# Performance work log

Measured on AMD Instinct MI355X. Metric: run time of the kernel, lower is better.

The kernel has to match this reference:

```python
import jax, jax.numpy as jnp
import numpy as np

N_HEADS = 16


def setup_inputs() -> dict:
    key = jax.random.key(0)
    k1, k2, k3 = jax.random.split(key, 3)
    d_model = 2048
    seq = 2048
    x = jax.random.normal(k1, (seq, d_model), dtype=jnp.float32)
    W_qkv = jax.random.normal(k2, (d_model, 3 * d_model), dtype=jnp.float32) * (d_model ** -0.5)
    b_qkv = jnp.zeros((3 * d_model,), dtype=jnp.float32)
    W_out = jax.random.normal(k3, (d_model, d_model), dtype=jnp.float32) * (d_model ** -0.5)
    b_out = jnp.zeros((d_model,), dtype=jnp.float32)
    return {"x": x, "W_qkv": W_qkv, "b_qkv": b_qkv, "W_out": W_out, "b_out": b_out}


def reference(x, W_qkv, b_qkv, W_out, b_out):
    seq, d_model = x.shape
    d_head = d_model // N_HEADS
    qkv = x @ W_qkv + b_qkv  # [seq, 3*d_model]
    q, k, v = jnp.split(qkv, 3, axis=1)
    # [seq, d_model] -> [n_heads, seq, d_head]
    split_heads = lambda t: t.reshape(seq, N_HEADS, d_head).transpose(1, 0, 2)
    q, k, v = split_heads(q), split_heads(k), split_heads(v)
    # NOTE: original module has NO 1/sqrt(d_head) scaling — kept faithful.
    attn = jnp.einsum('hqd,hkd->hqk', q, k)
    causal = jnp.arange(seq)[:, None] >= jnp.arange(seq)[None, :]
    attn = jnp.where(causal, attn, -jnp.inf)
    probs = jax.nn.softmax(attn, axis=-1)
    out = jnp.einsum('hqk,hkd->hqd', probs, v)  # [n_heads, seq, d_head]
    out = out.transpose(1, 0, 2).reshape(seq, d_model)
    return out @ W_out + b_out
```

## Files before the change

kernel.cpp:

```cpp
#include <hip/hip_runtime.h>
#include <stdint.h>

typedef __attribute__((ext_vector_type(8))) __bf16 bf16x8;
typedef __attribute__((ext_vector_type(4))) float  f32x4;

#define MFMA16(A, B, C) __builtin_amdgcn_mfma_f32_16x16x32_bf16((A), (B), (C), 0, 0, 0)

__device__ __forceinline__ unsigned short f2b(float f) {
  union { float f; uint32_t u; } c; c.f = f;
  uint32_t u = c.u;
  u += 0x7fffu + ((u >> 16) & 1u);
  return (unsigned short)(u >> 16);
}
__device__ __forceinline__ float b2f(unsigned short s) {
  union { uint32_t u; float f; } c; c.u = ((uint32_t)s) << 16;
  return c.f;
}
__device__ __forceinline__ void async_cp16(const void* g, void* l) {
  __builtin_amdgcn_global_load_lds((const __attribute__((address_space(1))) uint32_t*)g,
                                   (__attribute__((address_space(3))) uint32_t*)l, 16, 0, 0);
}

__global__ __launch_bounds__(256) void split_hi_lo(const float* __restrict__ in,
                                                   unsigned short* __restrict__ hi,
                                                   unsigned short* __restrict__ lo, int n4) {
  int i = blockIdx.x * 256 + threadIdx.x;
  if (i >= n4) return;
  const float4 v = ((const float4*)in)[i];
  float f[4] = {v.x, v.y, v.z, v.w};
  unsigned short hs[4], ls[4];
#pragma unroll
  for (int j = 0; j < 4; ++j) {
    hs[j] = f2b(f[j]);
    ls[j] = f2b(f[j] - b2f(hs[j]));
  }
  ((ushort4*)hi)[i] = make_ushort4(hs[0], hs[1], hs[2], hs[3]);
  ((ushort4*)lo)[i] = make_ushort4(ls[0], ls[1], ls[2], ls[3]);
}

template <int WLO>
__global__ __launch_bounds__(256) void transpose_split(const float* __restrict__ src,
                                                       unsigned short* __restrict__ dh,
                                                       unsigned short* __restrict__ dl,
                                                       int rows, int cols) {
  __shared__ float tile[64][65];
  const int r0 = blockIdx.y * 64, c0 = blockIdx.x * 64;
  const int t = threadIdx.x;
#pragma unroll
  for (int i = 0; i < 4; ++i) {
    int c = i * 256 + t;
    int rr = c >> 4, cc = (c & 15) << 2;
    const float4 v = *(const float4*)(src + (size_t)(r0 + rr) * cols + c0 + cc);
    tile[rr][cc] = v.x; tile[rr][cc + 1] = v.y; tile[rr][cc + 2] = v.z; tile[rr][cc + 3] = v.w;
  }
  __syncthreads();
#pragma unroll
  for (int i = 0; i < 4; ++i) {
    int c = i * 256 + t;
    int rr = c >> 4, cc = (c & 15) << 2;
    unsigned short hs[4], ls[4];
#pragma unroll
    for (int j = 0; j < 4; ++j) {
      float v = tile[cc + j][rr];
      hs[j] = f2b(v);
      ls[j] = f2b(v - b2f(hs[j]));
    }
    *(ushort4*)(dh + (size_t)(c0 + rr) * rows + r0 + cc) = make_ushort4(hs[0], hs[1], hs[2], hs[3]);
    if (WLO)
      *(ushort4*)(dl + (size_t)(c0 + rr) * rows + r0 + cc) = make_ushort4(ls[0], ls[1], ls[2], ls[3]);
  }
}

template <int NW, int EPI>
__global__ __launch_bounds__(NW * 64, 2) void gemm_bf16(
    const unsigned short* __restrict__ Ah, const unsigned short* __restrict__ Al,
    const unsigned short* __restrict__ Bh,
    const float* __restrict__ bias,
    void* __restrict__ o0, void* __restrict__ o1, void* __restrict__ o2, void* __restrict__ o3,
    void* __restrict__ o4) {
  constexpr int K = 2048;
  constexpr int NBUFA = (EPI == 1) ? 2 : 1;
  constexpr int WN = (NW == 8) ? 4 : 2;
  constexpr int WM = NW / WN;
  constexpr int MI = (128 / WM) / 16;
  constexpr int NI = (128 / WN) / 16;
  __shared__ unsigned short sA[NBUFA][128 * 32];
  __shared__ unsigned short sB[128 * 32];
  const int tid = threadIdx.x;
  const int wave = tid >> 6, lane = tid & 63;
  const int l16 = lane & 15, lq = lane >> 4;
  const int wr = wave / WN, wc = wave % WN;
  const int m0 = blockIdx.y * 128, n0 = blockIdx.x * 128;
  const bool two = (EPI == 1) && (n0 < 4096);

  f32x4 acc[MI][NI] = {};

  for (int k0 = 0; k0 < K; k0 += 32) {
#pragma unroll
    for (int i = 0; i < 512 / (NW * 64); ++i) {
      int c = i * (NW * 64) + tid;
      int row = c >> 2, cc = c & 3;
      int gcol = ((cc ^ ((row >> 1) & 3)) << 3);
      size_t ga = (size_t)(m0 + row) * K + k0 + gcol;
      size_t gb = (size_t)(n0 + row) * K + k0 + gcol;
      async_cp16(Ah + ga, sA[0] + c * 8);
      async_cp16(Bh + gb, sB + c * 8);
      if constexpr (EPI == 1) {
        if (two) async_cp16(Al + ga, sA[1] + c * 8);
      }
    }
    __syncthreads();

    bf16x8 ah[MI], al[MI], bh[NI];
#pragma unroll
    for (int mi = 0; mi < MI; ++mi) {
      int row = wr * (MI * 16) + mi * 16 + l16;
      int off = row * 32 + ((lq ^ ((row >> 1) & 3)) << 3);
      ah[mi] = *(const bf16x8*)(sA[0] + off);
      if constexpr (EPI == 1) {
        if (two) al[mi] = *(const bf16x8*)(sA[1] + off);
      }
    }
#pragma unroll
    for (int ni = 0; ni < NI; ++ni) {
      int row = wc * (NI * 16) + ni * 16 + l16;
      int off = row * 32 + ((lq ^ ((row >> 1) & 3)) << 3);
      bh[ni] = *(const bf16x8*)(sB + off);
    }
#pragma unroll
    for (int mi = 0; mi < MI; ++mi)
#pragma unroll
      for (int ni = 0; ni < NI; ++ni) {
        acc[mi][ni] = MFMA16(ah[mi], bh[ni], acc[mi][ni]);
        if constexpr (EPI == 1) {
          if (two) acc[mi][ni] = MFMA16(al[mi], bh[ni], acc[mi][ni]);
        }
      }
    __syncthreads();
  }

#pragma unroll
  for (int mi = 0; mi < MI; ++mi) {
#pragma unroll
    for (int ni = 0; ni < NI; ++ni) {
      int row = m0 + wr * (MI * 16) + mi * 16 + lq * 4;
      int col = n0 + wc * (NI * 16) + ni * 16 + l16;
      float bv = bias[col];
      if constexpr (EPI == 0) {
        float* C = (float*)o0;
#pragma unroll
        for (int r = 0; r < 4; ++r)
          C[(size_t)(row + r) * 2048 + col] = acc[mi][ni][r] + bv;
      } else {
        if (col < 4096) {
          unsigned short* dh; unsigned short* dl; int cc;
          if (col < 2048) { dh = (unsigned short*)o0; dl = (unsigned short*)o1; cc = col; }
          else            { dh = (unsigned short*)o2; dl = (unsigned short*)o3; cc = col - 2048; }
#pragma unroll
          for (int r = 0; r < 4; ++r) {
            float v = acc[mi][ni][r] + bv;
            unsigned short h = f2b(v);
            unsigned short l = f2b(v - b2f(h));
            dh[(size_t)(row + r) * 2048 + cc] = h;
            dl[(size_t)(row + r) * 2048 + cc] = l;
          }
        } else {
          unsigned short* vt = (unsigned short*)o4;
          unsigned short hs[4];
#pragma unroll
          for (int r = 0; r < 4; ++r) hs[r] = f2b(acc[mi][ni][r] + bv);
          *(ushort4*)(vt + (size_t)(col - 4096) * 2048 + row) = make_ushort4(hs[0], hs[1], hs[2], hs[3]);
        }
      }
    }
  }
}

__global__ __launch_bounds__(256, 2) void attn_fwd(
    const unsigned short* __restrict__ Qh, const unsigned short* __restrict__ Ql,
    const unsigned short* __restrict__ Kh,
    const unsigned short* __restrict__ Vt, unsigned short* __restrict__ aout) {
  const int head = blockIdx.y;
  const int x = blockIdx.x;
  const int qt = (head < 8) ? x : (31 - x);
  const int tid = threadIdx.x;
  const int wave = tid >> 6, lane = tid & 63;
  const int l16 = lane & 15, lq = lane >> 4;

  __shared__ unsigned short sKh[64 * 128];
  __shared__ unsigned short sV[128 * 64];
  __shared__ unsigned short sP[4][16 * 72];

  const int q0 = qt * 64 + wave * 16;

  bf16x8 qh[4], ql[4];
#pragma unroll
  for (int kc = 0; kc < 4; ++kc) {
    size_t off = (size_t)(q0 + l16) * 2048 + head * 128 + kc * 32 + lq * 8;
    qh[kc] = *(const bf16x8*)(Qh + off);
    ql[kc] = *(const bf16x8*)(Ql + off);
  }

  f32x4 o[8] = {};
  float mst = -1e30f, lst = 0.f;

  const int ktmax = qt + 1;
  for (int kt = 0; kt < ktmax; ++kt) {
#pragma unroll
    for (int i = 0; i < 4; ++i) {
      int c = i * 256 + tid;
      {
        int row = c >> 4, cc = c & 15;
        int gc = ((cc ^ (row & 7)) << 3);
        size_t g = (size_t)(kt * 64 + row) * 2048 + head * 128 + gc;
        async_cp16(Kh + g, sKh + c * 8);
      }
      {
        int row = c >> 3, cc = c & 7;
        int gc = ((cc ^ (row & 7)) << 3);
        size_t g = (size_t)(head * 128 + row) * 2048 + kt * 64 + gc;
        async_cp16(Vt + g, sV + c * 8);
      }
    }
    __syncthreads();

    f32x4 s[4] = {};
    __builtin_amdgcn_s_setprio(1);
#pragma unroll
    for (int kc = 0; kc < 4; ++kc) {
#pragma unroll
      for (int nk = 0; nk < 4; ++nk) {
        int krow = nk * 16 + l16;
        int off = krow * 128 + ((((kc << 2) + lq) ^ (krow & 7)) << 3);
        bf16x8 kbh = *(const bf16x8*)(sKh + off);
        s[nk] = MFMA16(kbh, qh[kc], s[nk]);
        s[nk] = MFMA16(kbh, ql[kc], s[nk]);
      }
    }
    __builtin_amdgcn_s_setprio(0);

    const int qg = q0 + l16;
    float pv[16];
    float mx = -1e30f;
#pragma unroll
    for (int nk = 0; nk < 4; ++nk)
#pragma unroll
      for (int r = 0; r < 4; ++r) {
        int kg = kt * 64 + nk * 16 + lq * 4 + r;
        float v = s[nk][r];
        if (kg > qg) v = -1e30f;
        pv[nk * 4 + r] = v;
        mx = fmaxf(mx, v);
      }
    mx = fmaxf(mx, __shfl_xor(mx, 16));
    mx = fmaxf(mx, __shfl_xor(mx, 32));
    float mnew = fmaxf(mst, mx);
    float scale = __expf(mst - mnew);
    float rsum = 0.f;
#pragma unroll
    for (int nk = 0; nk < 4; ++nk) {
      unsigned short pb[4];
#pragma unroll
      for (int r = 0; r < 4; ++r) {
        pb[r] = f2b(__expf(pv[nk * 4 + r] - mnew));
        rsum += b2f(pb[r]);
      }
      *(ushort4*)(&sP[wave][l16 * 72 + nk * 16 + lq * 4]) = make_ushort4(pb[0], pb[1], pb[2], pb[3]);
    }
    rsum += __shfl_xor(rsum, 16);
    rsum += __shfl_xor(rsum, 32);
    lst = lst * scale + rsum;
    mst = mnew;
#pragma unroll
    for (int nd = 0; nd < 8; ++nd) {
      o[nd][0] *= scale; o[nd][1] *= scale; o[nd][2] *= scale; o[nd][3] *= scale;
    }

    __builtin_amdgcn_s_setprio(1);
#pragma unroll
    for (int kc2 = 0; kc2 < 2; ++kc2) {
      bf16x8 pb = *(const bf16x8*)(&sP[wave][l16 * 72 + kc2 * 32 + lq * 8]);
#pragma unroll
      for (int nd = 0; nd < 8; ++nd) {
        int vrow = nd * 16 + l16;
        int off = vrow * 64 + ((((kc2 << 2) + lq) ^ (vrow & 7)) << 3);
        bf16x8 vb = *(const bf16x8*)(sV + off);
        o[nd] = MFMA16(vb, pb, o[nd]);
      }
    }
    __builtin_amdgcn_s_setprio(0);
    __syncthreads();
  }

  const float norm = 1.f / lst;
#pragma unroll
  for (int nd = 0; nd < 8; ++nd) {
    unsigned short hs[4];
#pragma unroll
    for (int r = 0; r < 4; ++r) hs[r] = f2b(o[nd][r] * norm);
    *(ushort4*)(aout + (size_t)(q0 + l16) * 2048 + head * 128 + nd * 16 + lq * 4) =
        make_ushort4(hs[0], hs[1], hs[2], hs[3]);
  }
}

extern "C" void kernel_launch(void* const* d_in, const int* in_sizes, int n_in,
                              void* d_out, int out_size, void* d_ws, size_t ws_size,
                              hipStream_t stream) {
  const float* x    = (const float*)d_in[0];
  const float* Wqkv = (const float*)d_in[1];
  const float* bqkv = (const float*)d_in[2];
  const float* Wout = (const float*)d_in[3];
  const float* bout = (const float*)d_in[4];
  float* out = (float*)d_out;

  unsigned short* w = (unsigned short*)d_ws;
  const size_t SZ = (size_t)2048 * 2048;
  unsigned short* xh  = w;  w += SZ;
  unsigned short* xl  = w;  w += SZ;
  unsigned short* wqh = w;  w += (size_t)6144 * 2048;
  unsigned short* wo  = w;  w += SZ;
  unsigned short* qh  = w;  w += SZ;
  unsigned short* ql  = w;  w += SZ;
  unsigned short* kh  = w;  w += SZ;
  unsigned short* kl  = w;  w += SZ;
  unsigned short* vt  = w;  w += SZ;
  unsigned short* ao  = w;  w += SZ;
  (void)ws_size; (void)in_sizes; (void)n_in; (void)out_size; (void)kl;

  split_hi_lo<<<4096, 256, 0, stream>>>(x, xh, xl, (int)(SZ / 4));
  transpose_split<0><<<dim3(96, 32), 256, 0, stream>>>(Wqkv, wqh, nullptr, 2048, 6144);
  transpose_split<0><<<dim3(32, 32), 256, 0, stream>>>(Wout, wo, nullptr, 2048, 2048);
  gemm_bf16<4, 1><<<dim3(48, 16), 256, 0, stream>>>(xh, xl, wqh, bqkv,
                                                    qh, ql, kh, kl, vt);
  attn_fwd<<<dim3(32, 16), 256, 0, stream>>>(qh, ql, kh, vt, ao);
  gemm_bf16<8, 0><<<dim3(16, 16), 512, 0, stream>>>(ao, nullptr, wo, bout, out,
                                                    nullptr, nullptr, nullptr, nullptr);
}
```

Measured before the change: 314.8 us.

## Merge preprocessing kernels into one launch and double GEMM K-tile to 64

Folds the x hi/lo split and both weight transpose-conversions into a single preprocess kernel, dispatched by block index, which removes two launches and their inter-kernel gaps. The GEMM K tile grows from 32 to 64, with a wider XOR swizzle and two inner k-steps per tile, which halves the number of barrier-separated load/compute iterations. The cost is double the LDS per block (about 48KB for the QKV GEMM with its lo buffer), which may reduce occupancy against the launch_bounds target of 2 blocks.

```diff
diff --git a/kernel.cpp b/kernel.cpp
--- a/kernel.cpp
+++ b/kernel.cpp
@@ -21,31 +21,11 @@
                                    (__attribute__((address_space(3))) uint32_t*)l, 16, 0, 0);
 }
 
-__global__ __launch_bounds__(256) void split_hi_lo(const float* __restrict__ in,
-                                                   unsigned short* __restrict__ hi,
-                                                   unsigned short* __restrict__ lo, int n4) {
-  int i = blockIdx.x * 256 + threadIdx.x;
-  if (i >= n4) return;
-  const float4 v = ((const float4*)in)[i];
-  float f[4] = {v.x, v.y, v.z, v.w};
-  unsigned short hs[4], ls[4];
-#pragma unroll
-  for (int j = 0; j < 4; ++j) {
-    hs[j] = f2b(f[j]);
-    ls[j] = f2b(f[j] - b2f(hs[j]));
-  }
-  ((ushort4*)hi)[i] = make_ushort4(hs[0], hs[1], hs[2], hs[3]);
-  ((ushort4*)lo)[i] = make_ushort4(ls[0], ls[1], ls[2], ls[3]);
-}
-
-template <int WLO>
-__global__ __launch_bounds__(256) void transpose_split(const float* __restrict__ src,
-                                                       unsigned short* __restrict__ dh,
-                                                       unsigned short* __restrict__ dl,
-                                                       int rows, int cols) {
-  __shared__ float tile[64][65];
-  const int r0 = blockIdx.y * 64, c0 = blockIdx.x * 64;
-  const int t = threadIdx.x;
+__device__ __forceinline__ void transpose_body(const float* __restrict__ src,
+                                               unsigned short* __restrict__ dh,
+                                               int rows, int cols, int bx, int by,
+                                               float (*tile)[65], int t) {
+  const int r0 = by * 64, c0 = bx * 64;
 #pragma unroll
   for (int i = 0; i < 4; ++i) {
     int c = i * 256 + t;
@@ -58,16 +38,38 @@
   for (int i = 0; i < 4; ++i) {
     int c = i * 256 + t;
     int rr = c >> 4, cc = (c & 15) << 2;
+    unsigned short hs[4];
+#pragma unroll
+    for (int j = 0; j < 4; ++j) hs[j] = f2b(tile[cc + j][rr]);
+    *(ushort4*)(dh + (size_t)(c0 + rr) * rows + r0 + cc) = make_ushort4(hs[0], hs[1], hs[2], hs[3]);
+  }
+}
+
+__global__ __launch_bounds__(256) void preprocess(
+    const float* __restrict__ x, unsigned short* __restrict__ xh, unsigned short* __restrict__ xl,
+    const float* __restrict__ Wqkv, unsigned short* __restrict__ wqh,
+    const float* __restrict__ Wout, unsigned short* __restrict__ wo) {
+  __shared__ float tile[64][65];
+  const int b = blockIdx.x;
+  const int t = threadIdx.x;
+  if (b < 4096) {
+    int i = b * 256 + t;
+    const float4 v = ((const float4*)x)[i];
+    float f[4] = {v.x, v.y, v.z, v.w};
     unsigned short hs[4], ls[4];
 #pragma unroll
     for (int j = 0; j < 4; ++j) {
-      float v = tile[cc + j][rr];
-      hs[j] = f2b(v);
-      ls[j] = f2b(v - b2f(hs[j]));
-    }
-    *(ushort4*)(dh + (size_t)(c0 + rr) * rows + r0 + cc) = make_ushort4(hs[0], hs[1], hs[2], hs[3]);
-    if (WLO)
-      *(ushort4*)(dl + (size_t)(c0 + rr) * rows + r0 + cc) = make_ushort4(ls[0], ls[1], ls[2], ls[3]);
+      hs[j] = f2b(f[j]);
+      ls[j] = f2b(f[j] - b2f(hs[j]));
+    }
+    ((ushort4*)xh)[i] = make_ushort4(hs[0], hs[1], hs[2], hs[3]);
+    ((ushort4*)xl)[i] = make_ushort4(ls[0], ls[1], ls[2], ls[3]);
+  } else if (b < 7168) {
+    int bb = b - 4096;
+    transpose_body(Wqkv, wqh, 2048, 6144, bb % 96, bb / 96, tile, t);
+  } else {
+    int bb = b - 7168;
+    transpose_body(Wout, wo, 2048, 2048, bb % 32, bb / 32, tile, t);
   }
 }
 
@@ -79,13 +81,14 @@
     void* __restrict__ o0, void* __restrict__ o1, void* __restrict__ o2, void* __restrict__ o3,
     void* __restrict__ o4) {
   constexpr int K = 2048;
+  constexpr int BK = 64;
   constexpr int NBUFA = (EPI == 1) ? 2 : 1;
   constexpr int WN = (NW == 8) ? 4 : 2;
   constexpr int WM = NW / WN;
   constexpr int MI = (128 / WM) / 16;
   constexpr int NI = (128 / WN) / 16;
-  __shared__ unsigned short sA[NBUFA][128 * 32];
-  __shared__ unsigned short sB[128 * 32];
+  __shared__ unsigned short sA[NBUFA][128 * BK];
+  __shared__ unsigned short sB[128 * BK];
   const int tid = threadIdx.x;
   const int wave = tid >> 6, lane = tid & 63;
   const int l16 = lane & 15, lq = lane >> 4;
@@ -95,12 +98,12 @@
 
   f32x4 acc[MI][NI] = {};
 
-  for (int k0 = 0; k0 < K; k0 += 32) {
-#pragma unroll
-    for (int i = 0; i < 512 / (NW * 64); ++i) {
+  for (int k0 = 0; k0 < K; k0 += BK) {
+#pragma unroll
+    for (int i = 0; i < 1024 / (NW * 64); ++i) {
       int c = i * (NW * 64) + tid;
-      int row = c >> 2, cc = c & 3;
-      int gcol = ((cc ^ ((row >> 1) & 3)) << 3);
+      int row = c >> 3, cc = c & 7;
+      int gcol = ((cc ^ (row & 7)) << 3);
       size_t ga = (size_t)(m0 + row) * K + k0 + gcol;
       size_t gb = (size_t)(n0 + row) * K + k0 + gcol;
       async_cp16(Ah + ga, sA[0] + c * 8);
@@ -111,31 +114,35 @@
     }
     __syncthreads();
 
-    bf16x8 ah[MI], al[MI], bh[NI];
-#pragma unroll
-    for (int mi = 0; mi < MI; ++mi) {
-      int row = wr * (MI * 16) + mi * 16 + l16;
-      int off = row * 32 + ((lq ^ ((row >> 1) & 3)) << 3);
-      ah[mi] = *(const bf16x8*)(sA[0] + off);
-      if constexpr (EPI == 1) {
-        if (two) al[mi] = *(const bf16x8*)(sA[1] + off);
-      }
-    }
-#pragma unroll
-    for (int ni = 0; ni < NI; ++ni) {
-      int row = wc * (NI * 16) + ni * 16 + l16;
-      int off = row * 32 + ((lq ^ ((row >> 1) & 3)) << 3);
-      bh[ni] = *(const bf16x8*)(sB + off);
-    }
-#pragma unroll
-    for (int mi = 0; mi < MI; ++mi)
+#pragma unroll
+    for (int kk = 0; kk < 2; ++kk) {
+      const int ci = (kk << 2) + lq;
+      bf16x8 ah[MI], al[MI], bh[NI];
+#pragma unroll
+      for (int mi = 0; mi < MI; ++mi) {
+        int row = wr * (MI * 16) + mi * 16 + l16;
+        int off = row * BK + ((ci ^ (row & 7)) << 3);
+        ah[mi] = *(const bf16x8*)(sA[0] + off);
+        if constexpr (EPI == 1) {
+          if (two) al[mi] = *(const bf16x8*)(sA[1] + off);
+        }
+      }
 #pragma unroll
       for (int ni = 0; ni < NI; ++ni) {
-        acc[mi][ni] = MFMA16(ah[mi], bh[ni], acc[mi][ni]);
-        if constexpr (EPI == 1) {
-          if (two) acc[mi][ni] = MFMA16(al[mi], bh[ni], acc[mi][ni]);
+        int row = wc * (NI * 16) + ni * 16 + l16;
+        int off = row * BK + ((ci ^ (row & 7)) << 3);
+        bh[ni] = *(const bf16x8*)(sB + off);
+      }
+#pragma unroll
+      for (int mi = 0; mi < MI; ++mi)
+#pragma unroll
+        for (int ni = 0; ni < NI; ++ni) {
+          acc[mi][ni] = MFMA16(ah[mi], bh[ni], acc[mi][ni]);
+          if constexpr (EPI == 1) {
+            if (two) acc[mi][ni] = MFMA16(al[mi], bh[ni], acc[mi][ni]);
+          }
         }
-      }
+    }
     __syncthreads();
   }
 
@@ -327,9 +334,7 @@
   unsigned short* ao  = w;  w += SZ;
   (void)ws_size; (void)in_sizes; (void)n_in; (void)out_size; (void)kl;
 
-  split_hi_lo<<<4096, 256, 0, stream>>>(x, xh, xl, (int)(SZ / 4));
-  transpose_split<0><<<dim3(96, 32), 256, 0, stream>>>(Wqkv, wqh, nullptr, 2048, 6144);
-  transpose_split<0><<<dim3(32, 32), 256, 0, stream>>>(Wout, wo, nullptr, 2048, 2048);
+  preprocess<<<8192, 256, 0, stream>>>(x, xh, xl, Wqkv, wqh, Wout, wo);
   gemm_bf16<4, 1><<<dim3(48, 16), 256, 0, stream>>>(xh, xl, wqh, bqkv,
                                                     qh, ql, kh, kl, vt);
   attn_fwd<<<dim3(32, 16), 256, 0, stream>>>(qh, ql, kh, vt, ao);
```

Measured after the change: 301.5 us. 4.2% less time.
